# Performance work log

Hardware: AMD Instinct MI355X
Metric: run time of the kernel (lower is better)

Reference implementation:

```python
import jax, jax.numpy as jnp
import numpy as np

D_MODEL = 1024
NUM_HEADS = 16
D_K = D_MODEL // NUM_HEADS


def setup_inputs() -> dict:
    key = jax.random.key(0)
    kq, kk, kv, k1, k2, k3, k4 = jax.random.split(key, 7)
    B, S = 2, 2048
    # Xavier-uniform init for square [d_model, d_model] weights
    limit = float(np.sqrt(6.0 / (D_MODEL + D_MODEL)))
    def xav(k):
        return jax.random.uniform(k, (D_MODEL, D_MODEL), jnp.float32, -limit, limit)
    return {
        "query": jax.random.normal(kq, (B, S, D_MODEL), jnp.float32),
        "key": jax.random.normal(kk, (B, S, D_MODEL), jnp.float32),
        "value": jax.random.normal(kv, (B, S, D_MODEL), jnp.float32),
        "W_q": xav(k1),
        "W_k": xav(k2),
        "W_v": xav(k3),
        "W_o": xav(k4),
    }


def reference(query, key, value, W_q, W_k, W_v, W_o):
    B, Sq, _ = query.shape
    Sk = key.shape[1]
    # Linear layers: y = x @ W.T (torch nn.Linear convention)
    Q = (query @ W_q.T).reshape(B, Sq, NUM_HEADS, D_K).transpose(0, 2, 1, 3)
    K = (key @ W_k.T).reshape(B, Sk, NUM_HEADS, D_K).transpose(0, 2, 1, 3)
    V = (value @ W_v.T).reshape(B, Sk, NUM_HEADS, D_K).transpose(0, 2, 1, 3)
    scale = 1.0 / jnp.sqrt(jnp.asarray(D_K, Q.dtype))
    scores = jnp.einsum("bhqd,bhkd->bhqk", Q, K) * scale  # [B,H,Sq,Sk]
    attn = jax.nn.softmax(scores, axis=-1)
    # dropout is identity in eval mode
    out = jnp.einsum("bhqk,bhkd->bhqd", attn, V)
    out = out.transpose(0, 2, 1, 3).reshape(B, Sq, D_MODEL)
    return out @ W_o.T
```

## Files before the change

### kernel.cpp

```cpp
#include <hip/hip_runtime.h>
#include <math.h>

typedef unsigned short ushort_t;
typedef __attribute__((ext_vector_type(8))) short short8;
typedef __attribute__((ext_vector_type(4))) float f32x4;
typedef __attribute__((ext_vector_type(4))) unsigned short ushort4v;
typedef __attribute__((ext_vector_type(2))) unsigned int uint2v;

#define D_MODEL 1024
#define SEQ 2048
#define MROWS 4096
#define PLANE (MROWS * D_MODEL)
#define WELEM (D_MODEL * D_MODEL)

static __device__ __forceinline__ ushort_t f2bf(float f) {
    unsigned u = __builtin_bit_cast(unsigned, f);
    return (ushort_t)((u + 0x7fffu + ((u >> 16) & 1u)) >> 16);
}
static __device__ __forceinline__ unsigned cvtpk(float lo, float hi) {
    unsigned r;
    asm("v_cvt_pk_bf16_f32 %0, %1, %2" : "=v"(r) : "v"(lo), "v"(hi));
    return r;
}

#define GLDS16(gp, lp)                                                         \
    __builtin_amdgcn_global_load_lds(                                          \
        (const __attribute__((address_space(1))) void*)(gp),                   \
        (__attribute__((address_space(3))) void*)(lp), 16, 0, 0)

__global__ __launch_bounds__(256)
void cvt_all(const float* __restrict__ q, const float* __restrict__ k,
             const float* __restrict__ v, const float* __restrict__ w0,
             const float* __restrict__ w1, const float* __restrict__ w2,
             const float* __restrict__ w3, ushort_t* __restrict__ dst) {
    int blk = blockIdx.x;
    const float* s;
    size_t base;
    if (blk < 6144) {
        const int p = blk >> 11;
        s = (p == 0) ? q : (p == 1) ? k : v;
        base = (size_t)p * PLANE;
        blk &= 2047;
    } else {
        const int p = (blk - 6144) >> 9;
        s = (p == 0) ? w0 : (p == 1) ? w1 : (p == 2) ? w2 : w3;
        base = 3 * (size_t)PLANE + (size_t)p * WELEM;
        blk = (blk - 6144) & 511;
    }
    const int i = (blk * 256 + threadIdx.x) * 8;
    float4 a = *(const float4*)(s + i);
    float4 bb = *(const float4*)(s + i + 4);
    short8 o;
    o[0] = (short)f2bf(a.x); o[1] = (short)f2bf(a.y);
    o[2] = (short)f2bf(a.z); o[3] = (short)f2bf(a.w);
    o[4] = (short)f2bf(bb.x); o[5] = (short)f2bf(bb.y);
    o[6] = (short)f2bf(bb.z); o[7] = (short)f2bf(bb.w);
    *(short8*)(dst + base + i) = o;
}

__global__ __launch_bounds__(256)
void gemm3(const ushort_t* __restrict__ Xq, const ushort_t* __restrict__ Wb,
           ushort_t* __restrict__ Cb) {
    __shared__ __align__(16) ushort_t As[128 * 64];
    __shared__ __align__(16) ushort_t Bs[128 * 64];

    const int z = blockIdx.z;
    const ushort_t* A = Xq + (size_t)z * PLANE;
    const ushort_t* B = Wb + (size_t)z * WELEM;
    ushort_t* C = Cb + (size_t)z * PLANE;

    const int tid = threadIdx.x;
    const int lane = tid & 63;
    const int wid = tid >> 6;
    const int wr = wid >> 1, wc = wid & 1;
    const int brow = blockIdx.y * 128;
    const int bcol = blockIdx.x * 128;

    const int lrow = lane >> 3;
    const int loff = ((lane & 7) ^ lrow) * 8;

    const ushort_t* aS[4];
    const ushort_t* bS[4];
#pragma unroll
    for (int i = 0; i < 4; ++i) {
        aS[i] = A + (size_t)(brow + wid * 32 + i * 8 + lrow) * D_MODEL + loff;
        bS[i] = B + (size_t)(bcol + wid * 32 + i * 8 + lrow) * D_MODEL + loff;
    }

    f32x4 acc[4][4];
#pragma unroll
    for (int i = 0; i < 4; ++i)
#pragma unroll
        for (int j = 0; j < 4; ++j) acc[i][j] = {0.f, 0.f, 0.f, 0.f};

    const int fr = lane & 15, fg = lane >> 4;

    for (int k0 = 0; k0 < D_MODEL; k0 += 64) {
        __syncthreads();
#pragma unroll
        for (int i = 0; i < 4; ++i) {
            GLDS16(aS[i] + k0, As + (wid * 32 + i * 8) * 64);
            GLDS16(bS[i] + k0, Bs + (wid * 32 + i * 8) * 64);
        }
        __syncthreads();
#pragma unroll
        for (int ks = 0; ks < 2; ++ks) {
            const int coff = (ks * 32 + fg * 8) ^ ((fr & 7) << 3);
            short8 af[4], bw[4];
#pragma unroll
            for (int mi = 0; mi < 4; ++mi)
                af[mi] = *(const short8*)&As[(wr * 64 + mi * 16 + fr) * 64 + coff];
#pragma unroll
            for (int nj = 0; nj < 4; ++nj)
                bw[nj] = *(const short8*)&Bs[(wc * 64 + nj * 16 + fr) * 64 + coff];
#pragma unroll
            for (int mi = 0; mi < 4; ++mi)
#pragma unroll
                for (int nj = 0; nj < 4; ++nj)
                    acc[mi][nj] = __builtin_amdgcn_mfma_f32_16x16x32_bf16(
                        af[mi], bw[nj], acc[mi][nj], 0, 0, 0);
        }
    }

    if (z < 2) {
#pragma unroll
        for (int mi = 0; mi < 4; ++mi)
#pragma unroll
            for (int nj = 0; nj < 4; ++nj) {
                const int n = bcol + wc * 64 + nj * 16 + fr;
#pragma unroll
                for (int r = 0; r < 4; ++r) {
                    const int m = brow + wr * 64 + mi * 16 + fg * 4 + r;
                    C[(size_t)m * D_MODEL + n] = f2bf(acc[mi][nj][r]);
                }
            }
    } else {
#pragma unroll
        for (int mi = 0; mi < 4; ++mi)
#pragma unroll
            for (int nj = 0; nj < 4; ++nj) {
                const int n = bcol + wc * 64 + nj * 16 + fr;
                const int m0 = brow + wr * 64 + mi * 16 + fg * 4;
                ushort4v o4;
#pragma unroll
                for (int r = 0; r < 4; ++r) o4[r] = f2bf(acc[mi][nj][r]);
                *(ushort4v*)&C[((size_t)(m0 >> 11) << 21) + (size_t)n * SEQ + (m0 & 2047)] = o4;
            }
    }
}

__global__ __launch_bounds__(256)
void gemm_out(const ushort_t* __restrict__ A, const ushort_t* __restrict__ B,
              float* __restrict__ C) {
    __shared__ __align__(16) ushort_t As[2][128 * 64];
    __shared__ __align__(16) ushort_t Bs[2][64 * 64];

    const int tid = threadIdx.x;
    const int lane = tid & 63;
    const int wid = tid >> 6;
    const int wr = wid >> 1, wc = wid & 1;
    const int brow = blockIdx.y * 128;
    const int bcol = blockIdx.x * 64;

    const int lrow = lane >> 3;
    const int loff = ((lane & 7) ^ lrow) * 8;

    const ushort_t* aSrc[4];
    const ushort_t* bSrc[2];
#pragma unroll
    for (int i = 0; i < 4; ++i)
        aSrc[i] = A + (size_t)(brow + (wid * 4 + i) * 8 + lrow) * D_MODEL + loff;
#pragma unroll
    for (int i = 0; i < 2; ++i)
        bSrc[i] = B + (size_t)(bcol + (wid * 2 + i) * 8 + lrow) * D_MODEL + loff;

    f32x4 acc[4][2];
#pragma unroll
    for (int i = 0; i < 4; ++i)
#pragma unroll
        for (int j = 0; j < 2; ++j) acc[i][j] = {0.f, 0.f, 0.f, 0.f};

    const int fr = lane & 15, fg = lane >> 4;

#pragma unroll
    for (int i = 0; i < 4; ++i) GLDS16(aSrc[i], As[0] + (wid * 4 + i) * 512);
#pragma unroll
    for (int i = 0; i < 2; ++i) GLDS16(bSrc[i], Bs[0] + (wid * 2 + i) * 512);

    int cur = 0;
    for (int k0 = 0; k0 < D_MODEL; k0 += 64) {
        __syncthreads();
        if (k0 + 64 < D_MODEL) {
#pragma unroll
            for (int i = 0; i < 4; ++i)
                GLDS16(aSrc[i] + k0 + 64, As[cur ^ 1] + (wid * 4 + i) * 512);
#pragma unroll
            for (int i = 0; i < 2; ++i)
                GLDS16(bSrc[i] + k0 + 64, Bs[cur ^ 1] + (wid * 2 + i) * 512);
        }
#pragma unroll
        for (int ks = 0; ks < 2; ++ks) {
            const int coff = (ks * 32 + fg * 8) ^ ((fr & 7) << 3);
            short8 af[4], bw[2];
#pragma unroll
            for (int mi = 0; mi < 4; ++mi)
                af[mi] = *(const short8*)&As[cur][(wr * 64 + mi * 16 + fr) * 64 + coff];
#pragma unroll
            for (int nj = 0; nj < 2; ++nj)
                bw[nj] = *(const short8*)&Bs[cur][(wc * 32 + nj * 16 + fr) * 64 + coff];
#pragma unroll
            for (int mi = 0; mi < 4; ++mi)
#pragma unroll
                for (int nj = 0; nj < 2; ++nj)
                    acc[mi][nj] = __builtin_amdgcn_mfma_f32_16x16x32_bf16(
                        af[mi], bw[nj], acc[mi][nj], 0, 0, 0);
        }
        cur ^= 1;
    }

#pragma unroll
    for (int mi = 0; mi < 4; ++mi)
#pragma unroll
        for (int nj = 0; nj < 2; ++nj) {
            const int n = bcol + wc * 32 + nj * 16 + fr;
#pragma unroll
            for (int r = 0; r < 4; ++r) {
                const int m = brow + wr * 64 + mi * 16 + fg * 4 + r;
                C[(size_t)m * D_MODEL + n] = acc[mi][nj][r];
            }
        }
}

__global__ __launch_bounds__(512)
void attn_mfma(const ushort_t* __restrict__ Qp, const ushort_t* __restrict__ Kp,
               const ushort_t* __restrict__ VT, ushort_t* __restrict__ Ap) {
    __shared__ __align__(16) ushort_t Ks[2][64 * 64];
    __shared__ __align__(16) ushort_t Vs[2][64 * 64];
    __shared__ __align__(16) ushort_t Ps[8 * 16 * 64];

    const int tid = threadIdx.x;
    const int lane = tid & 63;
    const int wid = tid >> 6;
    const int bid = blockIdx.x;
    const int qt = bid & 15;
    const int h = (bid >> 4) & 15;
    const int b = bid >> 8;

    const int lrow = lane >> 3;
    const int loff = ((lane & 7) ^ lrow) * 8;
    const int fr = lane & 15, fg = lane >> 4;

    const int m0 = b * SEQ + qt * 128;

#pragma unroll
    for (int j = 0; j < 2; ++j) {
        const ushort_t* qS =
            Qp + (size_t)(m0 + wid * 16 + j * 8 + lrow) * D_MODEL + h * 64 + loff;
        GLDS16(qS, Ps + (wid * 16 + j * 8) * 64);
    }
    const ushort_t* kS =
        Kp + (size_t)(b * SEQ + wid * 8 + lrow) * D_MODEL + h * 64 + loff;
    const ushort_t* vS =
        VT + ((size_t)b << 21) + (size_t)(h * 64 + wid * 8 + lrow) * SEQ + loff;
    GLDS16(kS, Ks[0] + wid * 512);
    GLDS16(vS, Vs[0] + wid * 512);
    kS += 64 * D_MODEL;
    vS += 64;
    __syncthreads();

    short8 aq[2];
#pragma unroll
    for (int ks = 0; ks < 2; ++ks)
        aq[ks] = *(const short8*)&Ps[(wid * 16 + fr) * 64 +
                                     ((ks * 32 + fg * 8) ^ ((fr & 7) << 3))];

    f32x4 accO[4];
#pragma unroll
    for (int nd = 0; nd < 4; ++nd) accO[nd] = {0.f, 0.f, 0.f, 0.f};
    float m_s = -INFINITY;
    float l_p = 0.f;

    const float CEXP = 0.18033688011112042f;
    const int pbase = wid * 1024 + fr * 64;

    int cur = 0;
    for (int kt = 0; kt < SEQ / 64; ++kt) {
        __syncthreads();
        if (kt + 1 < SEQ / 64) {
            GLDS16(kS, Ks[cur ^ 1] + wid * 512);
            GLDS16(vS, Vs[cur ^ 1] + wid * 512);
            kS += 64 * D_MODEL;
            vS += 64;
        }

        f32x4 accS[4];
#pragma unroll
        for (int n = 0; n < 4; ++n) accS[n] = {0.f, 0.f, 0.f, 0.f};
        __builtin_amdgcn_s_setprio(1);
#pragma unroll
        for (int ks = 0; ks < 2; ++ks) {
            const int coff = (ks * 32 + fg * 8) ^ ((fr & 7) << 3);
#pragma unroll
            for (int n = 0; n < 4; ++n) {
                short8 ak = *(const short8*)&Ks[cur][(n * 16 + fr) * 64 + coff];
                accS[n] = __builtin_amdgcn_mfma_f32_16x16x32_bf16(ak, aq[ks],
                                                                  accS[n], 0, 0, 0);
            }
        }
        __builtin_amdgcn_s_setprio(0);

        float mx = accS[0][0];
#pragma unroll
        for (int n = 0; n < 4; ++n)
#pragma unroll
            for (int r = 0; r < 4; ++r) mx = fmaxf(mx, accS[n][r]);
        mx = fmaxf(mx, __shfl_xor(mx, 16));
        mx = fmaxf(mx, __shfl_xor(mx, 32));
        const float cand = mx * CEXP;
        if (__any(cand > m_s + 8.f)) {
            const float mnew = fmaxf(m_s, cand);
            const float al = __builtin_amdgcn_exp2f(m_s - mnew);
            m_s = mnew;
            l_p *= al;
#pragma unroll
            for (int r = 0; r < 4; ++r) {
                const float ar = __shfl(al, (lane & 48) | (fg * 4 + r));
#pragma unroll
                for (int nd = 0; nd < 4; ++nd) accO[nd][r] *= ar;
            }
        }
        float ps = 0.f;
        const float nm = -m_s;
#pragma unroll
        for (int n = 0; n < 4; ++n)
#pragma unroll
            for (int r = 0; r < 4; ++r) {
                const float p = __builtin_amdgcn_exp2f(fmaf(accS[n][r], CEXP, nm));
                accS[n][r] = p;
                ps += p;
            }
        l_p += ps;

#pragma unroll
        for (int n = 0; n < 4; ++n) {
            uint2v pw2 = {cvtpk(accS[n][0], accS[n][1]),
                          cvtpk(accS[n][2], accS[n][3])};
            const int w = (n * 4 + fg) ^ (fr & 14);
            *(uint2v*)&Ps[pbase + w * 4] = pw2;
        }

        __builtin_amdgcn_s_setprio(1);
#pragma unroll
        for (int ks = 0; ks < 2; ++ks) {
            const int coff = (ks * 32 + fg * 8) ^ ((fr & 7) << 3);
            const int p0 = (ks * 8 + 2 * fg) ^ (fr & 14);
            short8 ap = *(const short8*)&Ps[pbase + p0 * 4];
#pragma unroll
            for (int nd = 0; nd < 4; ++nd) {
                short8 bv = *(const short8*)&Vs[cur][(nd * 16 + fr) * 64 + coff];
                accO[nd] = __builtin_amdgcn_mfma_f32_16x16x32_bf16(ap, bv,
                                                                   accO[nd], 0, 0, 0);
            }
        }
        __builtin_amdgcn_s_setprio(0);
        cur ^= 1;
    }

    float lt = l_p;
    lt += __shfl_xor(lt, 16);
    lt += __shfl_xor(lt, 32);
#pragma unroll
    for (int r = 0; r < 4; ++r) {
        const float lq = __shfl(lt, (lane & 48) | (fg * 4 + r));
        const float inv = 1.0f / lq;
        const int row = m0 + wid * 16 + fg * 4 + r;
#pragma unroll
        for (int nd = 0; nd < 4; ++nd)
            Ap[(size_t)row * D_MODEL + h * 64 + nd * 16 + fr] =
                f2bf(accO[nd][r] * inv);
    }
}

extern "C" void kernel_launch(void* const* d_in, const int* in_sizes, int n_in,
                              void* d_out, int out_size, void* d_ws, size_t ws_size,
                              hipStream_t stream) {
    const float* query = (const float*)d_in[0];
    const float* key   = (const float*)d_in[1];
    const float* value = (const float*)d_in[2];
    const float* W_q   = (const float*)d_in[3];
    const float* W_k   = (const float*)d_in[4];
    const float* W_v   = (const float*)d_in[5];
    const float* W_o   = (const float*)d_in[6];
    float* out = (float*)d_out;

    ushort_t* ws = (ushort_t*)d_ws;
    ushort_t* Xq = ws;
    ushort_t* Wb = ws + 3 * (size_t)PLANE;
    ushort_t* Qp = ws + 4 * (size_t)PLANE;
    ushort_t* Kp = Qp + (size_t)PLANE;
    ushort_t* VT = Kp + (size_t)PLANE;
    ushort_t* Ap = VT + (size_t)PLANE;

    cvt_all<<<8192, 256, 0, stream>>>(query, key, value, W_q, W_k, W_v, W_o, Xq);

    dim3 g3(D_MODEL / 128, MROWS / 128, 3);
    gemm3<<<g3, 256, 0, stream>>>(Xq, Wb, Qp);

    attn_mfma<<<512, 512, 0, stream>>>(Qp, Kp, VT, Ap);

    dim3 go(D_MODEL / 64, MROWS / 128);
    gemm_out<<<go, 256, 0, stream>>>(Ap, Wb + 3 * (size_t)WELEM, out);
}
```

Measured before the change: 137.0 us.

## Use 32x32 MFMA in attention with register-resident P and retile output GEMM

The attention kernel moves from 16x16x32 to 32x32x16 bf16 MFMA, using 4 waves with 32 query rows each instead of 8 waves with 16 rows. The probability tile is packed in registers through v_permlane32_swap, which removes the LDS round trip for P. Output is staged through LDS so global stores are 16-byte and coalesced. The output projection GEMM becomes 128x128 tiles with a single LDS buffer and two barriers per k-step, dropping double buffering. This trades prefetch overlap in that GEMM for larger tiles and fewer blocks.

```diff
diff --git a/kernel.cpp b/kernel.cpp
--- a/kernel.cpp
+++ b/kernel.cpp
@@ -4,8 +4,10 @@
 typedef unsigned short ushort_t;
 typedef __attribute__((ext_vector_type(8))) short short8;
 typedef __attribute__((ext_vector_type(4))) float f32x4;
+typedef __attribute__((ext_vector_type(16))) float f32x16;
 typedef __attribute__((ext_vector_type(4))) unsigned short ushort4v;
 typedef __attribute__((ext_vector_type(2))) unsigned int uint2v;
+typedef __attribute__((ext_vector_type(4))) unsigned int uint4v;
 
 #define D_MODEL 1024
 #define SEQ 2048
@@ -150,79 +152,69 @@
 }
 
 __global__ __launch_bounds__(256)
-void gemm_out(const ushort_t* __restrict__ A, const ushort_t* __restrict__ B,
-              float* __restrict__ C) {
-    __shared__ __align__(16) ushort_t As[2][128 * 64];
-    __shared__ __align__(16) ushort_t Bs[2][64 * 64];
+void gemm_wo(const ushort_t* __restrict__ A, const ushort_t* __restrict__ B,
+             float* __restrict__ C) {
+    __shared__ __align__(16) ushort_t As[128 * 64];
+    __shared__ __align__(16) ushort_t Bs[128 * 64];
 
     const int tid = threadIdx.x;
     const int lane = tid & 63;
     const int wid = tid >> 6;
     const int wr = wid >> 1, wc = wid & 1;
     const int brow = blockIdx.y * 128;
-    const int bcol = blockIdx.x * 64;
+    const int bcol = blockIdx.x * 128;
 
     const int lrow = lane >> 3;
     const int loff = ((lane & 7) ^ lrow) * 8;
 
-    const ushort_t* aSrc[4];
-    const ushort_t* bSrc[2];
+    const ushort_t* aS[4];
+    const ushort_t* bS[4];
+#pragma unroll
+    for (int i = 0; i < 4; ++i) {
+        aS[i] = A + (size_t)(brow + wid * 32 + i * 8 + lrow) * D_MODEL + loff;
+        bS[i] = B + (size_t)(bcol + wid * 32 + i * 8 + lrow) * D_MODEL + loff;
+    }
+
+    f32x4 acc[4][4];
 #pragma unroll
     for (int i = 0; i < 4; ++i)
-        aSrc[i] = A + (size_t)(brow + (wid * 4 + i) * 8 + lrow) * D_MODEL + loff;
-#pragma unroll
-    for (int i = 0; i < 2; ++i)
-        bSrc[i] = B + (size_t)(bcol + (wid * 2 + i) * 8 + lrow) * D_MODEL + loff;
-
-    f32x4 acc[4][2];
-#pragma unroll
-    for (int i = 0; i < 4; ++i)
-#pragma unroll
-        for (int j = 0; j < 2; ++j) acc[i][j] = {0.f, 0.f, 0.f, 0.f};
+#pragma unroll
+        for (int j = 0; j < 4; ++j) acc[i][j] = {0.f, 0.f, 0.f, 0.f};
 
     const int fr = lane & 15, fg = lane >> 4;
 
-#pragma unroll
-    for (int i = 0; i < 4; ++i) GLDS16(aSrc[i], As[0] + (wid * 4 + i) * 512);
-#pragma unroll
-    for (int i = 0; i < 2; ++i) GLDS16(bSrc[i], Bs[0] + (wid * 2 + i) * 512);
-
-    int cur = 0;
     for (int k0 = 0; k0 < D_MODEL; k0 += 64) {
         __syncthreads();
-        if (k0 + 64 < D_MODEL) {
-#pragma unroll
-            for (int i = 0; i < 4; ++i)
-                GLDS16(aSrc[i] + k0 + 64, As[cur ^ 1] + (wid * 4 + i) * 512);
-#pragma unroll
-            for (int i = 0; i < 2; ++i)
-                GLDS16(bSrc[i] + k0 + 64, Bs[cur ^ 1] + (wid * 2 + i) * 512);
-        }
+#pragma unroll
+        for (int i = 0; i < 4; ++i) {
+            GLDS16(aS[i] + k0, As + (wid * 32 + i * 8) * 64);
+            GLDS16(bS[i] + k0, Bs + (wid * 32 + i * 8) * 64);
+        }
+        __syncthreads();
 #pragma unroll
         for (int ks = 0; ks < 2; ++ks) {
             const int coff = (ks * 32 + fg * 8) ^ ((fr & 7) << 3);
-            short8 af[4], bw[2];
+            short8 af[4], bw[4];
 #pragma unroll
             for (int mi = 0; mi < 4; ++mi)
-                af[mi] = *(const short8*)&As[cur][(wr * 64 + mi * 16 + fr) * 64 + coff];
-#pragma unroll
-            for (int nj = 0; nj < 2; ++nj)
-                bw[nj] = *(const short8*)&Bs[cur][(wc * 32 + nj * 16 + fr) * 64 + coff];
+                af[mi] = *(const short8*)&As[(wr * 64 + mi * 16 + fr) * 64 + coff];
+#pragma unroll
+            for (int nj = 0; nj < 4; ++nj)
+                bw[nj] = *(const short8*)&Bs[(wc * 64 + nj * 16 + fr) * 64 + coff];
 #pragma unroll
             for (int mi = 0; mi < 4; ++mi)
 #pragma unroll
-                for (int nj = 0; nj < 2; ++nj)
+                for (int nj = 0; nj < 4; ++nj)
                     acc[mi][nj] = __builtin_amdgcn_mfma_f32_16x16x32_bf16(
                         af[mi], bw[nj], acc[mi][nj], 0, 0, 0);
         }
-        cur ^= 1;
     }
 
 #pragma unroll
     for (int mi = 0; mi < 4; ++mi)
 #pragma unroll
-        for (int nj = 0; nj < 2; ++nj) {
-            const int n = bcol + wc * 32 + nj * 16 + fr;
+        for (int nj = 0; nj < 4; ++nj) {
+            const int n = bcol + wc * 64 + nj * 16 + fr;
 #pragma unroll
             for (int r = 0; r < 4; ++r) {
                 const int m = brow + wr * 64 + mi * 16 + fg * 4 + r;
@@ -231,12 +223,12 @@
         }
 }
 
-__global__ __launch_bounds__(512)
+__global__ __launch_bounds__(256)
 void attn_mfma(const ushort_t* __restrict__ Qp, const ushort_t* __restrict__ Kp,
                const ushort_t* __restrict__ VT, ushort_t* __restrict__ Ap) {
     __shared__ __align__(16) ushort_t Ks[2][64 * 64];
     __shared__ __align__(16) ushort_t Vs[2][64 * 64];
-    __shared__ __align__(16) ushort_t Ps[8 * 16 * 64];
+    __shared__ __align__(16) ushort_t Qs[128 * 64];
 
     const int tid = threadIdx.x;
     const int lane = tid & 63;
@@ -248,73 +240,83 @@
 
     const int lrow = lane >> 3;
     const int loff = ((lane & 7) ^ lrow) * 8;
-    const int fr = lane & 15, fg = lane >> 4;
+    const int q31 = lane & 31;
+    const int hi = lane >> 5;
 
     const int m0 = b * SEQ + qt * 128;
 
 #pragma unroll
+    for (int j = 0; j < 4; ++j) {
+        const ushort_t* qS =
+            Qp + (size_t)(m0 + wid * 32 + j * 8 + lrow) * D_MODEL + h * 64 + loff;
+        GLDS16(qS, Qs + (wid * 32 + j * 8) * 64);
+    }
+    const ushort_t* kS[2];
+    const ushort_t* vS[2];
+#pragma unroll
     for (int j = 0; j < 2; ++j) {
-        const ushort_t* qS =
-            Qp + (size_t)(m0 + wid * 16 + j * 8 + lrow) * D_MODEL + h * 64 + loff;
-        GLDS16(qS, Ps + (wid * 16 + j * 8) * 64);
-    }
-    const ushort_t* kS =
-        Kp + (size_t)(b * SEQ + wid * 8 + lrow) * D_MODEL + h * 64 + loff;
-    const ushort_t* vS =
-        VT + ((size_t)b << 21) + (size_t)(h * 64 + wid * 8 + lrow) * SEQ + loff;
-    GLDS16(kS, Ks[0] + wid * 512);
-    GLDS16(vS, Vs[0] + wid * 512);
-    kS += 64 * D_MODEL;
-    vS += 64;
+        const int cr = wid * 16 + j * 8 + lrow;
+        kS[j] = Kp + (size_t)(b * SEQ + cr) * D_MODEL + h * 64 + loff;
+        vS[j] = VT + ((size_t)b << 21) + (size_t)(h * 64 + cr) * SEQ + loff;
+        GLDS16(kS[j], Ks[0] + (wid * 16 + j * 8) * 64);
+        GLDS16(vS[j], Vs[0] + (wid * 16 + j * 8) * 64);
+        kS[j] += 64 * D_MODEL;
+        vS[j] += 64;
+    }
     __syncthreads();
 
-    short8 aq[2];
-#pragma unroll
-    for (int ks = 0; ks < 2; ++ks)
-        aq[ks] = *(const short8*)&Ps[(wid * 16 + fr) * 64 +
-                                     ((ks * 32 + fg * 8) ^ ((fr & 7) << 3))];
-
-    f32x4 accO[4];
-#pragma unroll
-    for (int nd = 0; nd < 4; ++nd) accO[nd] = {0.f, 0.f, 0.f, 0.f};
+    const int qrow = wid * 32 + q31;
+    const int rsw = (q31 & 7);
+    short8 aq[4];
+#pragma unroll
+    for (int s = 0; s < 4; ++s)
+        aq[s] = *(const short8*)&Qs[qrow * 64 + (((s * 2 + hi) ^ rsw) * 8)];
+
+    f32x16 accO[2];
+#pragma unroll
+    for (int db = 0; db < 2; ++db)
+#pragma unroll
+        for (int r = 0; r < 16; ++r) accO[db][r] = 0.f;
     float m_s = -INFINITY;
     float l_p = 0.f;
 
     const float CEXP = 0.18033688011112042f;
-    const int pbase = wid * 1024 + fr * 64;
 
     int cur = 0;
     for (int kt = 0; kt < SEQ / 64; ++kt) {
         __syncthreads();
         if (kt + 1 < SEQ / 64) {
-            GLDS16(kS, Ks[cur ^ 1] + wid * 512);
-            GLDS16(vS, Vs[cur ^ 1] + wid * 512);
-            kS += 64 * D_MODEL;
-            vS += 64;
-        }
-
-        f32x4 accS[4];
-#pragma unroll
-        for (int n = 0; n < 4; ++n) accS[n] = {0.f, 0.f, 0.f, 0.f};
+#pragma unroll
+            for (int j = 0; j < 2; ++j) {
+                GLDS16(kS[j], Ks[cur ^ 1] + (wid * 16 + j * 8) * 64);
+                GLDS16(vS[j], Vs[cur ^ 1] + (wid * 16 + j * 8) * 64);
+                kS[j] += 64 * D_MODEL;
+                vS[j] += 64;
+            }
+        }
+
+        f32x16 accS[2];
+#pragma unroll
+        for (int kb = 0; kb < 2; ++kb)
+#pragma unroll
+            for (int r = 0; r < 16; ++r) accS[kb][r] = 0.f;
         __builtin_amdgcn_s_setprio(1);
 #pragma unroll
-        for (int ks = 0; ks < 2; ++ks) {
-            const int coff = (ks * 32 + fg * 8) ^ ((fr & 7) << 3);
-#pragma unroll
-            for (int n = 0; n < 4; ++n) {
-                short8 ak = *(const short8*)&Ks[cur][(n * 16 + fr) * 64 + coff];
-                accS[n] = __builtin_amdgcn_mfma_f32_16x16x32_bf16(ak, aq[ks],
-                                                                  accS[n], 0, 0, 0);
-            }
-        }
+        for (int s = 0; s < 4; ++s)
+#pragma unroll
+            for (int kb = 0; kb < 2; ++kb) {
+                short8 ak = *(const short8*)&Ks[cur][(kb * 32 + q31) * 64 +
+                                                     (((s * 2 + hi) ^ rsw) * 8)];
+                accS[kb] = __builtin_amdgcn_mfma_f32_32x32x16_bf16(
+                    ak, aq[s], accS[kb], 0, 0, 0);
+            }
         __builtin_amdgcn_s_setprio(0);
 
         float mx = accS[0][0];
 #pragma unroll
-        for (int n = 0; n < 4; ++n)
-#pragma unroll
-            for (int r = 0; r < 4; ++r) mx = fmaxf(mx, accS[n][r]);
-        mx = fmaxf(mx, __shfl_xor(mx, 16));
+        for (int kb = 0; kb < 2; ++kb)
+#pragma unroll
+            for (int r = 0; r < 16; ++r) mx = fmaxf(mx, accS[kb][r]);
         mx = fmaxf(mx, __shfl_xor(mx, 32));
         const float cand = mx * CEXP;
         if (__any(cand > m_s + 8.f)) {
@@ -323,61 +325,75 @@
             m_s = mnew;
             l_p *= al;
 #pragma unroll
-            for (int r = 0; r < 4; ++r) {
-                const float ar = __shfl(al, (lane & 48) | (fg * 4 + r));
-#pragma unroll
-                for (int nd = 0; nd < 4; ++nd) accO[nd][r] *= ar;
-            }
+            for (int db = 0; db < 2; ++db)
+#pragma unroll
+                for (int r = 0; r < 16; ++r) accO[db][r] *= al;
         }
         float ps = 0.f;
         const float nm = -m_s;
 #pragma unroll
-        for (int n = 0; n < 4; ++n)
-#pragma unroll
-            for (int r = 0; r < 4; ++r) {
-                const float p = __builtin_amdgcn_exp2f(fmaf(accS[n][r], CEXP, nm));
-                accS[n][r] = p;
+        for (int kb = 0; kb < 2; ++kb)
+#pragma unroll
+            for (int r = 0; r < 16; ++r) {
+                const float p = __builtin_amdgcn_exp2f(fmaf(accS[kb][r], CEXP, nm));
+                accS[kb][r] = p;
                 ps += p;
             }
         l_p += ps;
 
-#pragma unroll
-        for (int n = 0; n < 4; ++n) {
-            uint2v pw2 = {cvtpk(accS[n][0], accS[n][1]),
-                          cvtpk(accS[n][2], accS[n][3])};
-            const int w = (n * 4 + fg) ^ (fr & 14);
-            *(uint2v*)&Ps[pbase + w * 4] = pw2;
+        short8 pf[4];
+#pragma unroll
+        for (int ks4 = 0; ks4 < 4; ++ks4) {
+            const int kb = ks4 >> 1;
+            const int bse = (ks4 & 1) * 8;
+            unsigned w0 = cvtpk(accS[kb][bse + 0], accS[kb][bse + 1]);
+            unsigned w1 = cvtpk(accS[kb][bse + 2], accS[kb][bse + 3]);
+            unsigned w2 = cvtpk(accS[kb][bse + 4], accS[kb][bse + 5]);
+            unsigned w3 = cvtpk(accS[kb][bse + 6], accS[kb][bse + 7]);
+            asm("v_permlane32_swap_b32 %0, %1" : "+v"(w0), "+v"(w2));
+            asm("v_permlane32_swap_b32 %0, %1" : "+v"(w1), "+v"(w3));
+            uint4v u = {w0, w1, w2, w3};
+            pf[ks4] = __builtin_bit_cast(short8, u);
         }
 
         __builtin_amdgcn_s_setprio(1);
 #pragma unroll
-        for (int ks = 0; ks < 2; ++ks) {
-            const int coff = (ks * 32 + fg * 8) ^ ((fr & 7) << 3);
-            const int p0 = (ks * 8 + 2 * fg) ^ (fr & 14);
-            short8 ap = *(const short8*)&Ps[pbase + p0 * 4];
-#pragma unroll
-            for (int nd = 0; nd < 4; ++nd) {
-                short8 bv = *(const short8*)&Vs[cur][(nd * 16 + fr) * 64 + coff];
-                accO[nd] = __builtin_amdgcn_mfma_f32_16x16x32_bf16(ap, bv,
-                                                                   accO[nd], 0, 0, 0);
-            }
-        }
+        for (int db = 0; db < 2; ++db)
+#pragma unroll
+            for (int ks4 = 0; ks4 < 4; ++ks4) {
+                short8 av = *(const short8*)&Vs[cur][(db * 32 + q31) * 64 +
+                                                     (((ks4 * 2 + hi) ^ rsw) * 8)];
+                accO[db] = __builtin_amdgcn_mfma_f32_32x32x16_bf16(
+                    av, pf[ks4], accO[db], 0, 0, 0);
+            }
         __builtin_amdgcn_s_setprio(0);
         cur ^= 1;
     }
 
-    float lt = l_p;
-    lt += __shfl_xor(lt, 16);
-    lt += __shfl_xor(lt, 32);
-#pragma unroll
-    for (int r = 0; r < 4; ++r) {
-        const float lq = __shfl(lt, (lane & 48) | (fg * 4 + r));
-        const float inv = 1.0f / lq;
-        const int row = m0 + wid * 16 + fg * 4 + r;
-#pragma unroll
-        for (int nd = 0; nd < 4; ++nd)
-            Ap[(size_t)row * D_MODEL + h * 64 + nd * 16 + fr] =
-                f2bf(accO[nd][r] * inv);
+    float lt = l_p + __shfl_xor(l_p, 32);
+    const float inv = 1.0f / lt;
+    unsigned* QsW = (unsigned*)Qs;
+    const int kkw = 2 * (q31 & 15);
+#pragma unroll
+    for (int db = 0; db < 2; ++db)
+#pragma unroll
+        for (int blk = 0; blk < 4; ++blk) {
+            const int c0 = 4 * blk + 2 * hi + 16 * db;
+            uint2v u;
+            u[0] = cvtpk(accO[db][4 * blk + 0] * inv, accO[db][4 * blk + 1] * inv);
+            u[1] = cvtpk(accO[db][4 * blk + 2] * inv, accO[db][4 * blk + 3] * inv);
+            *(uint2v*)&QsW[qrow * 32 + (c0 ^ kkw)] = u;
+        }
+    __syncthreads();
+#pragma unroll
+    for (int pass = 0; pass < 4; ++pass) {
+        const int r = wid * 32 + pass * 8 + (lane >> 3);
+        const int g8 = lane & 7;
+        const int kk = 2 * (r & 15);
+        uint2v u0 = *(const uint2v*)&QsW[r * 32 + ((4 * g8) ^ kk)];
+        uint2v u1 = *(const uint2v*)&QsW[r * 32 + ((4 * g8 + 2) ^ kk)];
+        uint4v o = {u0[0], u0[1], u1[0], u1[1]};
+        *(uint4v*)&Ap[(size_t)(m0 + r) * D_MODEL + h * 64 + g8 * 8] = o;
     }
 }
 
@@ -406,8 +422,8 @@
     dim3 g3(D_MODEL / 128, MROWS / 128, 3);
     gemm3<<<g3, 256, 0, stream>>>(Xq, Wb, Qp);
 
-    attn_mfma<<<512, 512, 0, stream>>>(Qp, Kp, VT, Ap);
-
-    dim3 go(D_MODEL / 64, MROWS / 128);
-    gemm_out<<<go, 256, 0, stream>>>(Ap, Wb + 3 * (size_t)WELEM, out);
-}
+    attn_mfma<<<512, 256, 0, stream>>>(Qp, Kp, VT, Ap);
+
+    dim3 go(D_MODEL / 128, MROWS / 128);
+    gemm_wo<<<go, 256, 0, stream>>>(Ap, Wb + 3 * (size_t)WELEM, out);
+}
```

Result: slower. 140.5 us (+2.6%).
